# Performance work log

Measured on AMD Instinct MI355X. Metric: run time of the kernel, lower is better.

The kernel has to match this reference:

```python
import jax, jax.numpy as jnp
import numpy as np

N_AGENTS = 512
OBS = 128          # embed_fc_input_size (args.obs_space)
INP = 656          # input_shape
HID = 64           # rnn_hidden_dim
LAT = 256          # latent_dim (hard-coded)
NH = 64            # NN_HIDDEN_SIZE (hard-coded)
VAR_FLOOR = 0.002
KL_W = 1e-4
H_W = 1e-4
SOFT_W = 1.0
BN_EPS = 1e-5
LOG2PI = float(np.log(2.0 * np.pi))


def _bn(x, g, b, axis):
    # BatchNorm1d in training mode: biased batch stats over `axis`
    m = x.mean(axis=axis, keepdims=True)
    v = x.var(axis=axis, keepdims=True)
    return g * (x - m) / jnp.sqrt(v + BN_EPS) + b


def setup_inputs() -> dict:
    key = jax.random.key(0)
    ks = jax.random.split(key, 12)
    s = 0.02  # small init so exp(log-var head) stays tame
    p = {}
    p["obs"] = jax.random.normal(ks[0], (N_AGENTS, INP), jnp.float32)
    p["hidden_state"] = jax.random.normal(ks[1], (N_AGENTS, HID), jnp.float32)
    p["eps"] = jax.random.normal(ks[2], (N_AGENTS, LAT), jnp.float32)

    def lin(k, din, dout):
        return jax.random.normal(k, (din, dout), jnp.float32) * s, jnp.zeros((dout,), jnp.float32)

    # embed_net: Linear(OBS,64) -> BN -> LeakyReLU -> Linear(64, 2*LAT)
    p["eW1"], p["eb1"] = lin(ks[3], OBS, NH)
    p["eg"], p["ebt"] = jnp.ones((NH,), jnp.float32), jnp.zeros((NH,), jnp.float32)
    p["eW2"], p["eb2"] = lin(ks[4], NH, 2 * LAT)
    # inference_net: Linear(HID+INP,64) -> BN -> LeakyReLU -> Linear(64, 2*LAT)
    p["iW1"], p["ib1"] = lin(ks[5], HID + INP, NH)
    p["ig"], p["ibt"] = jnp.ones((NH,), jnp.float32), jnp.zeros((NH,), jnp.float32)
    p["iW2"], p["ib2"] = lin(ks[6], NH, 2 * LAT)
    # dis_net: Linear(2*LAT,64) -> BN -> LeakyReLU -> Linear(64,1)
    p["dW1"], p["db1"] = lin(ks[7], 2 * LAT, NH)
    p["dg"], p["dbt"] = jnp.ones((NH,), jnp.float32), jnp.zeros((NH,), jnp.float32)
    p["dW2"], p["db2"] = lin(ks[8], NH, 1)
    return p


def reference(obs, hidden_state, eps,
              eW1, eb1, eg, ebt, eW2, eb2,
              iW1, ib1, ig, ibt, iW2, ib2,
              dW1, db1, dg, dbt, dW2, db2):
    n = N_AGENTS  # bs == 1 is hard-coded in the module
    # --- embed_net ---
    emb_in = obs[:, -OBS:]
    h = jax.nn.leaky_relu(_bn(emb_in @ eW1 + eb1, eg, ebt, axis=0))
    lat = h @ eW2 + eb2                       # [n, 2*LAT]
    mu = lat[:, :LAT]
    var = jnp.maximum(jnp.exp(lat[:, LAT:]), VAR_FLOOR)
    sig = jnp.sqrt(var)
    latent = mu + sig * eps                   # rsample

    # --- inference_net (h_in detached) ---
    inf_in = jnp.concatenate([jax.lax.stop_gradient(hidden_state), obs], axis=1)
    hi = jax.nn.leaky_relu(_bn(inf_in @ iW1 + ib1, ig, ibt, axis=0))
    li = hi @ iW2 + ib2
    mu_q = li[:, :LAT]
    var_q = jnp.maximum(jnp.exp(li[:, LAT:]), VAR_FLOOR)
    sig_q = jnp.sqrt(var_q)

    entropy = (0.5 + 0.5 * LOG2PI + jnp.log(sig)).sum(-1).mean()
    kl = (jnp.log(sig_q / sig) + (var + (mu - mu_q) ** 2) / (2.0 * var_q) - 0.5).sum(-1).mean()
    loss0 = jnp.minimum(entropy * H_W + kl * KL_W, 2000.0)
    ce_loss = jnp.log1p(jnp.exp(loss0))

    # --- vectorized ring-shift pairwise pass (replaces n_agents Python loop) ---
    shifts = jnp.arange(1, n + 1)                        # loop iterations 1..n
    idx = (jnp.arange(n)[None, :] - shifts[:, None]) % n  # [n_shifts, n]
    moved = latent[idx]                                   # [S, n, LAT]

    # mi: per-dim Normal(mu_j, sig_j).log_prob of shifted latents
    logp = -((moved - mu[None]) ** 2) / (2.0 * var[None]) - jnp.log(sig)[None] - 0.5 * LOG2PI
    mi = jnp.maximum(logp + 13.9, -13.9).sum(-1) / LAT    # [S, n]

    # dis_net on concat(latent_j, moved_{s,j}); BN stats per shift iteration (batch = n)
    pair = jnp.concatenate([jnp.broadcast_to(latent[None], (n, n, LAT)), moved], axis=-1)
    h1 = pair @ dW1 + db1                                 # [S, n, NH]
    h1 = jax.nn.leaky_relu(_bn(h1, dg, dbt, axis=1))
    dis = jnp.abs(h1 @ dW2 + db2)[..., 0]                 # [S, n]

    mi_cat = mi.reshape(1, -1)                            # shift-major, matches cat order
    dis_cat = dis.reshape(1, -1)

    mi_n = (mi_cat - mi_cat.min(1, keepdims=True)) / (mi_cat.max(1, keepdims=True) - mi_cat.min(1, keepdims=True) + 1e-12)
    dis_n = (dis_cat - dis_cat.min(1, keepdims=True)) / (dis_cat.max(1, keepdims=True) - dis_cat.min(1, keepdims=True) + 1e-12)

    dis_loss = -jnp.minimum(mi_n + dis_n, 1.0).sum() / n  # / bs / n_agents, bs=1
    dis_norm = jnp.abs(dis_n).sum(axis=1).sum() / n
    c_dis_loss = (dis_norm + SOFT_W * dis_loss) / n
    loss = ce_loss + c_dis_loss
    return loss, c_dis_loss, ce_loss
```

## Files before the change

### kernel.cpp

```cpp
#include <hip/hip_runtime.h>

#define LOG2PI_F 1.8378770664093453f

#define W_ENC_PRE 0
#define W_INF_PRE 32768
#define W_ACC     65536
#define W_FIN     65792
#define W_MIMM    65796
#define W_DSMM    66308
#define W_ENT     67332
#define W_KL      67588
#define W_LATENT  67844
#define W_RPC     198916
#define W_A       723204
#define W_B       755972
#define W_AT      788740
#define W_BT      821508
#define W_ALPHA   854276
#define W_BETA    887044
#define W_MI      919812
#define W_DIS     1181956

__global__ __launch_bounds__(256) void k_pre(
    const float* __restrict__ obs, const float* __restrict__ hid,
    const float* __restrict__ eW1, const float* __restrict__ iW1,
    float* __restrict__ enc_pre, float* __restrict__ inf_pre,
    float* __restrict__ acc) {
  __shared__ float x[2][720];
  __shared__ float pi[4][2][64];
  __shared__ float pe[4][2][64];
  const int t = threadIdx.x;
  const int i0 = blockIdx.x * 2;
#pragma unroll
  for (int r = 0; r < 2; ++r)
    for (int k = t; k < 720; k += 256)
      x[r][k] = (k < 64) ? hid[(i0 + r) * 64 + k] : obs[(i0 + r) * 656 + (k - 64)];
  __syncthreads();
  const int c = t & 63, q = t >> 6;
  {
    float a0 = 0.f, a1 = 0.f;
    const int k0 = q * 180;
    for (int k = k0; k < k0 + 180; ++k) {
      const float w = iW1[k * 64 + c];
      a0 = fmaf(x[0][k], w, a0);
      a1 = fmaf(x[1][k], w, a1);
    }
    pi[q][0][c] = a0;
    pi[q][1][c] = a1;
  }
  {
    float a0 = 0.f, a1 = 0.f;
    const int k0 = q * 32;
    for (int k = k0; k < k0 + 32; ++k) {
      const float w = eW1[k * 64 + c];
      a0 = fmaf(x[0][592 + k], w, a0);
      a1 = fmaf(x[1][592 + k], w, a1);
    }
    pe[q][0][c] = a0;
    pe[q][1][c] = a1;
  }
  __syncthreads();
  if (t < 128) {
    const int r = t >> 6, c2 = t & 63;
    const float s = pi[0][r][c2] + pi[1][r][c2] + pi[2][r][c2] + pi[3][r][c2];
    inf_pre[(i0 + r) * 64 + c2] = s;
    atomicAdd(&acc[128 + c2], s);
    atomicAdd(&acc[192 + c2], s * s);
  } else {
    const int r = (t >> 6) & 1, c2 = t & 63;
    const float s = pe[0][r][c2] + pe[1][r][c2] + pe[2][r][c2] + pe[3][r][c2];
    enc_pre[(i0 + r) * 64 + c2] = s;
    atomicAdd(&acc[c2], s);
    atomicAdd(&acc[64 + c2], s * s);
  }
}

__global__ __launch_bounds__(256) void k_lat(
    const float* __restrict__ enc_pre, const float* __restrict__ inf_pre,
    const float* __restrict__ acc, const float* __restrict__ eg,
    const float* __restrict__ ebt, const float* __restrict__ ig,
    const float* __restrict__ ibt, const float* __restrict__ eW2,
    const float* __restrict__ eb2, const float* __restrict__ iW2,
    const float* __restrict__ ib2, const float* __restrict__ eps,
    float* __restrict__ latent, float* __restrict__ rpc,
    float* __restrict__ ent_part, float* __restrict__ kl_part) {
  __shared__ float sc[2][64], sh[2][64];
  __shared__ float h[2][2][64];
  __shared__ float red[256];
  const int t = threadIdx.x;
  const int i0 = blockIdx.x * 2;
  if (t < 128) {
    const int w = t >> 6, c = t & 63;
    const float sum = acc[w * 128 + c], sq = acc[w * 128 + 64 + c];
    const float mean = sum * (1.f / 512.f);
    float var = sq * (1.f / 512.f) - mean * mean;
    var = fmaxf(var, 0.f);
    const float g = w ? ig[c] : eg[c];
    const float bt = w ? ibt[c] : ebt[c];
    const float scale = g * rsqrtf(var + 1e-5f);
    sc[w][c] = scale;
    sh[w][c] = bt - mean * scale;
  }
  __syncthreads();
  {
    const int w = t >> 7, r = (t >> 6) & 1, c = t & 63;
    const float* pre = w ? inf_pre : enc_pre;
    const float v = fmaf(pre[(i0 + r) * 64 + c], sc[w][c], sh[w][c]);
    h[w][r][c] = (v >= 0.f) ? v : 0.01f * v;
  }
  __syncthreads();
  float me[2] = {0.f, 0.f}, ve[2] = {0.f, 0.f};
  float mq[2] = {0.f, 0.f}, vq[2] = {0.f, 0.f};
  for (int c = 0; c < 64; ++c) {
    const float we1 = eW2[c * 512 + t], we2 = eW2[c * 512 + 256 + t];
    const float wi1 = iW2[c * 512 + t], wi2 = iW2[c * 512 + 256 + t];
#pragma unroll
    for (int r = 0; r < 2; ++r) {
      me[r] = fmaf(h[0][r][c], we1, me[r]);
      ve[r] = fmaf(h[0][r][c], we2, ve[r]);
      mq[r] = fmaf(h[1][r][c], wi1, mq[r]);
      vq[r] = fmaf(h[1][r][c], wi2, vq[r]);
    }
  }
  const float ebm = eb2[t], ebv = eb2[256 + t];
  const float ibm = ib2[t], ibv = ib2[256 + t];
  float ent_l = 0.f, kl_l = 0.f;
#pragma unroll
  for (int r = 0; r < 2; ++r) {
    const int i = i0 + r;
    const float m = me[r] + ebm;
    const float var = fmaxf(expf(ve[r] + ebv), 0.002f);
    const float lse = 0.5f * logf(var);
    const float sig = sqrtf(var);
    const float mqq = mq[r] + ibm;
    const float varq = fmaxf(expf(vq[r] + ibv), 0.002f);
    const float lsq = 0.5f * logf(varq);
    latent[i * 256 + t] = fmaf(sig, eps[i * 256 + t], m);
    const float r_ = sqrtf(0.5f / var);
    float4 o;
    o.x = r_;
    o.y = m * r_;
    o.z = 13.9f - 0.5f * LOG2PI_F - lse;
    o.w = 0.f;
    *(float4*)&rpc[(i * 256 + t) * 4] = o;
    ent_l += 0.5f + 0.5f * LOG2PI_F + lse;
    const float dmu = m - mqq;
    kl_l += lsq - lse + (var + dmu * dmu) * (0.5f / varq) - 0.5f;
  }
  red[t] = ent_l;
  __syncthreads();
  for (int o = 128; o; o >>= 1) {
    if (t < o) red[t] += red[t + o];
    __syncthreads();
  }
  if (t == 0) ent_part[blockIdx.x] = red[0];
  __syncthreads();
  red[t] = kl_l;
  __syncthreads();
  for (int o = 128; o; o >>= 1) {
    if (t < o) red[t] += red[t + o];
    __syncthreads();
  }
  if (t == 0) kl_part[blockIdx.x] = red[0];
}

__global__ __launch_bounds__(256) void k_AB(
    const float* __restrict__ latent, const float* __restrict__ dW1,
    float* __restrict__ A, float* __restrict__ B, float* __restrict__ At,
    float* __restrict__ Bt, float* __restrict__ fin) {
  if (blockIdx.x == 0 && threadIdx.x == 0) {
    fin[0] = 0.f;
    fin[1] = 0.f;
    ((unsigned*)fin)[2] = 0u;
  }
  __shared__ float ls[2][256];
  __shared__ float pA[4][2][64], pB[4][2][64];
  const int t = threadIdx.x;
  const int j0 = blockIdx.x * 2;
  ls[0][t] = latent[j0 * 256 + t];
  ls[1][t] = latent[(j0 + 1) * 256 + t];
  __syncthreads();
  const int c = t & 63, q = t >> 6;
  float aA0 = 0.f, aA1 = 0.f, aB0 = 0.f, aB1 = 0.f;
  const int k0 = q * 64;
  for (int k = k0; k < k0 + 64; ++k) {
    const float wA = dW1[k * 64 + c];
    const float wB = dW1[(256 + k) * 64 + c];
    aA0 = fmaf(ls[0][k], wA, aA0);
    aA1 = fmaf(ls[1][k], wA, aA1);
    aB0 = fmaf(ls[0][k], wB, aB0);
    aB1 = fmaf(ls[1][k], wB, aB1);
  }
  pA[q][0][c] = aA0;
  pA[q][1][c] = aA1;
  pB[q][0][c] = aB0;
  pB[q][1][c] = aB1;
  __syncthreads();
  if (t < 128) {
    const int r = t >> 6, c2 = t & 63;
    const float s = pA[0][r][c2] + pA[1][r][c2] + pA[2][r][c2] + pA[3][r][c2];
    A[(j0 + r) * 64 + c2] = s;
    At[c2 * 512 + j0 + r] = s;
  } else {
    const int r = (t >> 6) & 1, c2 = t & 63;
    const float s = pB[0][r][c2] + pB[1][r][c2] + pB[2][r][c2] + pB[3][r][c2];
    B[(j0 + r) * 64 + c2] = s;
    Bt[c2 * 512 + j0 + r] = s;
  }
}

__global__ __launch_bounds__(256) void k_cross(
    const float* __restrict__ At, const float* __restrict__ Bt,
    const float* __restrict__ dg, const float* __restrict__ dbt,
    float* __restrict__ alpha, float* __restrict__ beta) {
  __shared__ float a[512], bb[512];
  __shared__ float red[256];
  __shared__ float pc[4][64];
  const int t = threadIdx.x;
  const int c = blockIdx.x >> 3;
  const int s0 = (blockIdx.x & 7) * 64;
  const float a0 = At[c * 512 + t], a1 = At[c * 512 + 256 + t];
  const float b0 = Bt[c * 512 + t], b1 = Bt[c * 512 + 256 + t];
  a[t] = a0;
  a[t + 256] = a1;
  bb[t] = b0;
  bb[t + 256] = b1;
  red[t] = a0 + a1 + b0 + b1;
  __syncthreads();
  for (int o = 128; o; o >>= 1) {
    if (t < o) red[t] += red[t + o];
    __syncthreads();
  }
  const float S = red[0];
  __syncthreads();
  red[t] = a0 * a0 + a1 * a1 + b0 * b0 + b1 * b1;
  __syncthreads();
  for (int o = 128; o; o >>= 1) {
    if (t < o) red[t] += red[t + o];
    __syncthreads();
  }
  const float Q = red[0];
  const int sl = t & 63, part = t >> 6;
  const int s = s0 + sl;
  float cr = 0.f;
  for (int j = part * 128; j < part * 128 + 128; ++j)
    cr = fmaf(a[j], bb[(j - s - 1) & 511], cr);
  pc[part][sl] = cr;
  __syncthreads();
  if (t < 64) {
    const int ss = s0 + t;
    const float cross = pc[0][t] + pc[1][t] + pc[2][t] + pc[3][t];
    const float mean = S * (1.f / 512.f);
    const float var = (Q + 2.f * cross) * (1.f / 512.f) - mean * mean;
    const float gc = dg[c], bc = dbt[c];
    const float al = rsqrtf(var + 1e-5f) * gc;
    alpha[ss * 64 + c] = al;
    beta[ss * 64 + c] = bc - mean * al;
  }
}

__global__ __launch_bounds__(256) void k_mi(
    const float* __restrict__ latent, const float* __restrict__ rpc,
    float* __restrict__ mi, float2* __restrict__ miMM) {
  __shared__ float lats[64][65];
  __shared__ float rpcs[16 * 256];
  __shared__ float mt[64][17];
  __shared__ float fmn[256], fmx[256];
  const int t = threadIdx.x;
  const int jt = blockIdx.x & 31, pt = blockIdx.x >> 5;
  const int j0 = jt * 16, p0 = pt * 64;
  const int pl = t & 31, jg = t >> 5;
  float regL[16], regR[16];
#pragma unroll
  for (int i = 0; i < 16; ++i) {
    const int idx = t + i * 256;
    regL[i] = latent[(p0 + (idx >> 6)) * 256 + (idx & 63)];
    regR[i] = rpc[(j0 + (idx >> 8)) * 1024 + (idx & 255)];
  }
  float a00 = 0.f, a01 = 0.f, a10 = 0.f, a11 = 0.f;
  for (int kc = 0; kc < 4; ++kc) {
    __syncthreads();
#pragma unroll
    for (int i = 0; i < 16; ++i) {
      const int idx = t + i * 256;
      lats[idx >> 6][idx & 63] = regL[i];
      rpcs[idx] = regR[i];
    }
    __syncthreads();
    if (kc < 3) {
#pragma unroll
      for (int i = 0; i < 16; ++i) {
        const int idx = t + i * 256;
        regL[i] = latent[(p0 + (idx >> 6)) * 256 + (kc + 1) * 64 + (idx & 63)];
        regR[i] = rpc[(j0 + (idx >> 8)) * 1024 + (kc + 1) * 256 + (idx & 255)];
      }
    }
    const float4* rp0 = (const float4*)&rpcs[(jg * 2) * 256];
    const float4* rp1 = (const float4*)&rpcs[(jg * 2 + 1) * 256];
#pragma unroll 8
    for (int k = 0; k < 64; ++k) {
      const float l0 = lats[pl][k], l1 = lats[pl + 32][k];
      const float4 r0 = rp0[k];
      const float4 r1 = rp1[k];
      float v;
      v = fmaf(l0, r0.x, -r0.y);
      a00 += fmaxf(fmaf(-v, v, r0.z), -13.9f);
      v = fmaf(l1, r0.x, -r0.y);
      a01 += fmaxf(fmaf(-v, v, r0.z), -13.9f);
      v = fmaf(l0, r1.x, -r1.y);
      a10 += fmaxf(fmaf(-v, v, r1.z), -13.9f);
      v = fmaf(l1, r1.x, -r1.y);
      a11 += fmaxf(fmaf(-v, v, r1.z), -13.9f);
    }
  }
  a00 *= (1.f / 256.f);
  a01 *= (1.f / 256.f);
  a10 *= (1.f / 256.f);
  a11 *= (1.f / 256.f);
  __syncthreads();
  mt[pl][jg * 2] = a00;
  mt[pl + 32][jg * 2] = a01;
  mt[pl][jg * 2 + 1] = a10;
  mt[pl + 32][jg * 2 + 1] = a11;
  fmn[t] = fminf(fminf(a00, a01), fminf(a10, a11));
  fmx[t] = fmaxf(fmaxf(a00, a01), fmaxf(a10, a11));
  __syncthreads();
  for (int o = 128; o; o >>= 1) {
    if (t < o) {
      fmn[t] = fminf(fmn[t], fmn[t + o]);
      fmx[t] = fmaxf(fmx[t], fmx[t + o]);
    }
    __syncthreads();
  }
  if (t == 0) miMM[blockIdx.x] = make_float2(fmn[0], fmx[0]);
  for (int i = t; i < 1024; i += 256) {
    const int pr = i >> 4, jc = i & 15;
    mi[(p0 + pr) * 512 + (j0 + jc)] = mt[pr][jc];
  }
}

__global__ __launch_bounds__(256) void k_dis(
    const float* __restrict__ A, const float* __restrict__ B,
    const float* __restrict__ alpha, const float* __restrict__ beta,
    const float* __restrict__ dW2, const float* __restrict__ db2,
    float* __restrict__ dis, float2* __restrict__ dsMM) {
  __shared__ float As[8 * 66];
  __shared__ float Bs[64 * 66];
  __shared__ float als[71 * 66];
  __shared__ float bes[71 * 66];
  __shared__ float w2s[64];
  __shared__ float dt[64][9];
  __shared__ float fmn[256], fmx[256];
  const int t = threadIdx.x;
  const int jt = blockIdx.x & 63, pt = blockIdx.x >> 6;
  const int j0 = jt * 8, p0 = pt * 64;
  for (int idx = t; idx < 8 * 64; idx += 256)
    As[(idx >> 6) * 66 + (idx & 63)] = A[(j0 + (idx >> 6)) * 64 + (idx & 63)];
  for (int idx = t; idx < 64 * 64; idx += 256)
    Bs[(idx >> 6) * 66 + (idx & 63)] = B[(p0 + (idx >> 6)) * 64 + (idx & 63)];
  for (int idx = t; idx < 71 * 64; idx += 256) {
    const int r = idx >> 6, c = idx & 63;
    const int s = (j0 - p0 - 64 + r) & 511;
    als[r * 66 + c] = alpha[s * 64 + c];
    bes[r * 66 + c] = beta[s * 64 + c];
  }
  if (t < 64) w2s[t] = dW2[t];
  const float db2v = db2[0];
  __syncthreads();
  const int pl = t & 31, jg = t >> 5;
  const int rb0 = jg - pl + 63;
  const int rb1 = jg - pl + 31;
  float acc0 = 0.f, acc1 = 0.f;
  for (int c = 0; c < 64; c += 2) {
    const float2 av = *(const float2*)&As[jg * 66 + c];
    const float2 bv0 = *(const float2*)&Bs[pl * 66 + c];
    const float2 bv1 = *(const float2*)&Bs[(pl + 32) * 66 + c];
    const float2 al0 = *(const float2*)&als[rb0 * 66 + c];
    const float2 al1 = *(const float2*)&als[rb1 * 66 + c];
    const float2 be0 = *(const float2*)&bes[rb0 * 66 + c];
    const float2 be1 = *(const float2*)&bes[rb1 * 66 + c];
    const float2 w = *(const float2*)&w2s[c];
    float v;
    v = fmaf(av.x + bv0.x, al0.x, be0.x);
    v = (v >= 0.f) ? v : 0.01f * v;
    acc0 = fmaf(v, w.x, acc0);
    v = fmaf(av.y + bv0.y, al0.y, be0.y);
    v = (v >= 0.f) ? v : 0.01f * v;
    acc0 = fmaf(v, w.y, acc0);
    v = fmaf(av.x + bv1.x, al1.x, be1.x);
    v = (v >= 0.f) ? v : 0.01f * v;
    acc1 = fmaf(v, w.x, acc1);
    v = fmaf(av.y + bv1.y, al1.y, be1.y);
    v = (v >= 0.f) ? v : 0.01f * v;
    acc1 = fmaf(v, w.y, acc1);
  }
  acc0 = fabsf(acc0 + db2v);
  acc1 = fabsf(acc1 + db2v);
  dt[pl][jg] = acc0;
  dt[pl + 32][jg] = acc1;
  fmn[t] = fminf(acc0, acc1);
  fmx[t] = fmaxf(acc0, acc1);
  __syncthreads();
  for (int o = 128; o; o >>= 1) {
    if (t < o) {
      fmn[t] = fminf(fmn[t], fmn[t + o]);
      fmx[t] = fmaxf(fmx[t], fmx[t + o]);
    }
    __syncthreads();
  }
  if (t == 0) dsMM[blockIdx.x] = make_float2(fmn[0], fmx[0]);
  for (int idx = t; idx < 512; idx += 256) {
    const int pr = idx >> 3, jc = idx & 7;
    dis[(p0 + pr) * 512 + (j0 + jc)] = dt[pr][jc];
  }
}

__global__ __launch_bounds__(256) void k_sumfin(
    const float* __restrict__ mi, const float* __restrict__ dis,
    const float2* __restrict__ miMM, const float2* __restrict__ dsMM,
    float* __restrict__ fin, const float* __restrict__ ent_part,
    const float* __restrict__ kl_part, float* __restrict__ out) {
  __shared__ float red1[256], red2[256], red3[256], red4[256];
  __shared__ int lastflag;
  const int t = threadIdx.x;
  {
    const float2 v = miMM[t];
    const float2 w0 = dsMM[t], w1 = dsMM[t + 256];
    red1[t] = v.x;
    red2[t] = v.y;
    red3[t] = fminf(w0.x, w1.x);
    red4[t] = fmaxf(w0.y, w1.y);
  }
  __syncthreads();
  for (int o = 128; o; o >>= 1) {
    if (t < o) {
      red1[t] = fminf(red1[t], red1[t + o]);
      red2[t] = fmaxf(red2[t], red2[t + o]);
      red3[t] = fminf(red3[t], red3[t + o]);
      red4[t] = fmaxf(red4[t], red4[t + o]);
    }
    __syncthreads();
  }
  const float mi_mn = red1[0], mi_mx = red2[0];
  const float d_mn = red3[0], d_mx = red4[0];
  __syncthreads();
  const float inv_mi = 1.f / (mi_mx - mi_mn + 1e-12f);
  const float inv_d = 1.f / (d_mx - d_mn + 1e-12f);
  float s1 = 0.f, s2 = 0.f;
  for (int i = blockIdx.x * 256 + t; i < 512 * 512; i += 65536) {
    const float mn_ = (mi[i] - mi_mn) * inv_mi;
    const float dn_ = (dis[i] - d_mn) * inv_d;
    s1 += fminf(mn_ + dn_, 1.0f);
    s2 += dn_;
  }
  red1[t] = s1;
  red2[t] = s2;
  __syncthreads();
  for (int o = 128; o; o >>= 1) {
    if (t < o) {
      red1[t] += red1[t + o];
      red2[t] += red2[t + o];
    }
    __syncthreads();
  }
  if (t == 0) {
    atomicAdd(&fin[0], red1[0]);
    atomicAdd(&fin[1], red2[0]);
    __threadfence();
    const unsigned old = atomicAdd((unsigned*)&fin[2], 1u);
    lastflag = (old == 255u) ? 1 : 0;
  }
  __syncthreads();
  if (!lastflag) return;
  red1[t] = ent_part[t];
  red2[t] = kl_part[t];
  __syncthreads();
  for (int o = 128; o; o >>= 1) {
    if (t < o) {
      red1[t] += red1[t + o];
      red2[t] += red2[t + o];
    }
    __syncthreads();
  }
  if (t == 0) {
    const float S1 = atomicAdd(&fin[0], 0.f);
    const float S2 = atomicAdd(&fin[1], 0.f);
    const double entropy = (double)red1[0] / 512.0;
    const double kl = (double)red2[0] / 512.0;
    double l0 = entropy * 1e-4 + kl * 1e-4;
    if (l0 > 2000.0) l0 = 2000.0;
    const double ce = log1p(exp(l0));
    const double dis_loss = -(double)S1 / 512.0;
    const double dis_norm = (double)S2 / 512.0;
    const double c_dis = (dis_norm + dis_loss) / 512.0;
    out[0] = (float)(ce + c_dis);
    out[1] = (float)c_dis;
    out[2] = (float)ce;
  }
}

extern "C" void kernel_launch(void* const* d_in, const int* in_sizes, int n_in,
                              void* d_out, int out_size, void* d_ws,
                              size_t ws_size, hipStream_t stream) {
  (void)in_sizes;
  (void)n_in;
  (void)out_size;
  (void)ws_size;
  const float* obs = (const float*)d_in[0];
  const float* hid = (const float*)d_in[1];
  const float* eps = (const float*)d_in[2];
  const float* eW1 = (const float*)d_in[3];
  const float* eg = (const float*)d_in[5];
  const float* ebt = (const float*)d_in[6];
  const float* eW2 = (const float*)d_in[7];
  const float* eb2 = (const float*)d_in[8];
  const float* iW1 = (const float*)d_in[9];
  const float* ig = (const float*)d_in[11];
  const float* ibt = (const float*)d_in[12];
  const float* iW2 = (const float*)d_in[13];
  const float* ib2 = (const float*)d_in[14];
  const float* dW1 = (const float*)d_in[15];
  const float* dg = (const float*)d_in[17];
  const float* dbt = (const float*)d_in[18];
  const float* dW2 = (const float*)d_in[19];
  const float* db2 = (const float*)d_in[20];
  float* ws = (float*)d_ws;
  float* out = (float*)d_out;

  hipMemsetAsync(ws + W_ACC, 0, 256 * sizeof(float), stream);

  k_pre<<<256, 256, 0, stream>>>(obs, hid, eW1, iW1, ws + W_ENC_PRE,
                                 ws + W_INF_PRE, ws + W_ACC);
  k_lat<<<256, 256, 0, stream>>>(ws + W_ENC_PRE, ws + W_INF_PRE, ws + W_ACC, eg,
                                 ebt, ig, ibt, eW2, eb2, iW2, ib2, eps,
                                 ws + W_LATENT, ws + W_RPC, ws + W_ENT,
                                 ws + W_KL);
  k_AB<<<256, 256, 0, stream>>>(ws + W_LATENT, dW1, ws + W_A, ws + W_B,
                                ws + W_AT, ws + W_BT, ws + W_FIN);
  k_cross<<<512, 256, 0, stream>>>(ws + W_AT, ws + W_BT, dg, dbt, ws + W_ALPHA,
                                   ws + W_BETA);
  k_mi<<<256, 256, 0, stream>>>(ws + W_LATENT, ws + W_RPC, ws + W_MI,
                                (float2*)(ws + W_MIMM));
  k_dis<<<512, 256, 0, stream>>>(ws + W_A, ws + W_B, ws + W_ALPHA, ws + W_BETA,
                                 dW2, db2, ws + W_DIS, (float2*)(ws + W_DSMM));
  k_sumfin<<<256, 256, 0, stream>>>(ws + W_MI, ws + W_DIS,
                                    (const float2*)(ws + W_MIMM),
                                    (const float2*)(ws + W_DSMM), ws + W_FIN,
                                    ws + W_ENT, ws + W_KL, out);
}
```

Baseline: 201.2 us.

## Replace BN stat atomics with per-block partials and merge mi/dis kernels

The first-layer BatchNorm statistics no longer go through global atomics on a memset-zeroed buffer. Each k_pre block now writes its own partial sums and sums of squares, and every k_lat block reduces all 256 partials itself. The independent mi and dis kernels are merged into one 768-block launch that picks its branch by block index and shares one carved-up shared-memory buffer. This drops a memset, the atomic contention and one kernel launch, and lets both workloads fill the GPU together. The cost is that each k_lat block now makes 256 redundant strided reads, and the merged kernel's shared-memory footprint is sized for the larger branch, which may limit occupancy.

```diff
diff --git a/kernel.cpp b/kernel.cpp
--- a/kernel.cpp
+++ b/kernel.cpp
@@ -4,7 +4,6 @@
 
 #define W_ENC_PRE 0
 #define W_INF_PRE 32768
-#define W_ACC     65536
 #define W_FIN     65792
 #define W_MIMM    65796
 #define W_DSMM    66308
@@ -20,17 +19,20 @@
 #define W_BETA    887044
 #define W_MI      919812
 #define W_DIS     1181956
+#define W_PACC    1446144
 
 __global__ __launch_bounds__(256) void k_pre(
     const float* __restrict__ obs, const float* __restrict__ hid,
     const float* __restrict__ eW1, const float* __restrict__ iW1,
     float* __restrict__ enc_pre, float* __restrict__ inf_pre,
-    float* __restrict__ acc) {
+    float* __restrict__ pacc) {
   __shared__ float x[2][720];
   __shared__ float pi[4][2][64];
   __shared__ float pe[4][2][64];
+  __shared__ float sb[256];
   const int t = threadIdx.x;
-  const int i0 = blockIdx.x * 2;
+  const int vb = blockIdx.x;
+  const int i0 = vb * 2;
 #pragma unroll
   for (int r = 0; r < 2; ++r)
     for (int k = t; k < 720; k += 256)
@@ -60,38 +62,54 @@
     pe[q][1][c] = a1;
   }
   __syncthreads();
+  float s;
   if (t < 128) {
     const int r = t >> 6, c2 = t & 63;
-    const float s = pi[0][r][c2] + pi[1][r][c2] + pi[2][r][c2] + pi[3][r][c2];
+    s = pi[0][r][c2] + pi[1][r][c2] + pi[2][r][c2] + pi[3][r][c2];
     inf_pre[(i0 + r) * 64 + c2] = s;
-    atomicAdd(&acc[128 + c2], s);
-    atomicAdd(&acc[192 + c2], s * s);
   } else {
     const int r = (t >> 6) & 1, c2 = t & 63;
-    const float s = pe[0][r][c2] + pe[1][r][c2] + pe[2][r][c2] + pe[3][r][c2];
+    s = pe[0][r][c2] + pe[1][r][c2] + pe[2][r][c2] + pe[3][r][c2];
     enc_pre[(i0 + r) * 64 + c2] = s;
-    atomicAdd(&acc[c2], s);
-    atomicAdd(&acc[64 + c2], s * s);
+  }
+  sb[t] = s;
+  __syncthreads();
+  if (t < 64) {
+    const float e0 = sb[128 + t], e1 = sb[192 + t];
+    pacc[vb * 256 + t] = e0 + e1;
+    pacc[vb * 256 + 64 + t] = e0 * e0 + e1 * e1;
+  } else if (t < 128) {
+    const int c2 = t - 64;
+    const float v0 = sb[c2], v1 = sb[64 + c2];
+    pacc[vb * 256 + 128 + c2] = v0 + v1;
+    pacc[vb * 256 + 192 + c2] = v0 * v0 + v1 * v1;
   }
 }
 
 __global__ __launch_bounds__(256) void k_lat(
     const float* __restrict__ enc_pre, const float* __restrict__ inf_pre,
-    const float* __restrict__ acc, const float* __restrict__ eg,
+    const float* __restrict__ pacc, const float* __restrict__ eg,
     const float* __restrict__ ebt, const float* __restrict__ ig,
     const float* __restrict__ ibt, const float* __restrict__ eW2,
     const float* __restrict__ eb2, const float* __restrict__ iW2,
     const float* __restrict__ ib2, const float* __restrict__ eps,
     float* __restrict__ latent, float* __restrict__ rpc,
     float* __restrict__ ent_part, float* __restrict__ kl_part) {
+  __shared__ float sval[256];
   __shared__ float sc[2][64], sh[2][64];
   __shared__ float h[2][2][64];
   __shared__ float red[256];
   const int t = threadIdx.x;
   const int i0 = blockIdx.x * 2;
+  {
+    float v = 0.f;
+    for (int b = 0; b < 256; ++b) v += pacc[b * 256 + t];
+    sval[t] = v;
+  }
+  __syncthreads();
   if (t < 128) {
     const int w = t >> 6, c = t & 63;
-    const float sum = acc[w * 128 + c], sq = acc[w * 128 + 64 + c];
+    const float sum = sval[w * 128 + c], sq = sval[w * 128 + 64 + c];
     const float mean = sum * (1.f / 512.f);
     float var = sq * (1.f / 512.f) - mean * mean;
     var = fmaxf(var, 0.f);
@@ -259,159 +277,163 @@
   }
 }
 
-__global__ __launch_bounds__(256) void k_mi(
+__global__ __launch_bounds__(256) void k_midis(
     const float* __restrict__ latent, const float* __restrict__ rpc,
-    float* __restrict__ mi, float2* __restrict__ miMM) {
-  __shared__ float lats[64][65];
-  __shared__ float rpcs[16 * 256];
-  __shared__ float mt[64][17];
-  __shared__ float fmn[256], fmx[256];
+    const float* __restrict__ A, const float* __restrict__ B,
+    const float* __restrict__ alpha, const float* __restrict__ beta,
+    const float* __restrict__ dW2, const float* __restrict__ db2,
+    float* __restrict__ mi, float* __restrict__ dis,
+    float2* __restrict__ miMM, float2* __restrict__ dsMM) {
+  __shared__ __align__(16) float sm[15276];
   const int t = threadIdx.x;
-  const int jt = blockIdx.x & 31, pt = blockIdx.x >> 5;
-  const int j0 = jt * 16, p0 = pt * 64;
-  const int pl = t & 31, jg = t >> 5;
-  float regL[16], regR[16];
-#pragma unroll
-  for (int i = 0; i < 16; ++i) {
-    const int idx = t + i * 256;
-    regL[i] = latent[(p0 + (idx >> 6)) * 256 + (idx & 63)];
-    regR[i] = rpc[(j0 + (idx >> 8)) * 1024 + (idx & 255)];
-  }
-  float a00 = 0.f, a01 = 0.f, a10 = 0.f, a11 = 0.f;
-  for (int kc = 0; kc < 4; ++kc) {
-    __syncthreads();
+  if (blockIdx.x < 256) {
+    float* lats = sm;
+    float* rpcs = sm + 4160;
+    float* mt = sm + 8256;
+    float* fmn = sm + 9344;
+    float* fmx = sm + 9600;
+    const int vb = blockIdx.x;
+    const int jt = vb & 31, pt = vb >> 5;
+    const int j0 = jt * 16, p0 = pt * 64;
+    const int pl = t & 31, jg = t >> 5;
+    float regL[16], regR[16];
 #pragma unroll
     for (int i = 0; i < 16; ++i) {
       const int idx = t + i * 256;
-      lats[idx >> 6][idx & 63] = regL[i];
-      rpcs[idx] = regR[i];
-    }
-    __syncthreads();
-    if (kc < 3) {
+      regL[i] = latent[(p0 + (idx >> 6)) * 256 + (idx & 63)];
+      regR[i] = rpc[(j0 + (idx >> 8)) * 1024 + (idx & 255)];
+    }
+    float a00 = 0.f, a01 = 0.f, a10 = 0.f, a11 = 0.f;
+    for (int kc = 0; kc < 4; ++kc) {
+      __syncthreads();
 #pragma unroll
       for (int i = 0; i < 16; ++i) {
         const int idx = t + i * 256;
-        regL[i] = latent[(p0 + (idx >> 6)) * 256 + (kc + 1) * 64 + (idx & 63)];
-        regR[i] = rpc[(j0 + (idx >> 8)) * 1024 + (kc + 1) * 256 + (idx & 255)];
+        lats[(idx >> 6) * 65 + (idx & 63)] = regL[i];
+        rpcs[idx] = regR[i];
       }
-    }
-    const float4* rp0 = (const float4*)&rpcs[(jg * 2) * 256];
-    const float4* rp1 = (const float4*)&rpcs[(jg * 2 + 1) * 256];
+      __syncthreads();
+      if (kc < 3) {
+#pragma unroll
+        for (int i = 0; i < 16; ++i) {
+          const int idx = t + i * 256;
+          regL[i] = latent[(p0 + (idx >> 6)) * 256 + (kc + 1) * 64 + (idx & 63)];
+          regR[i] = rpc[(j0 + (idx >> 8)) * 1024 + (kc + 1) * 256 + (idx & 255)];
+        }
+      }
+      const float4* rp0 = (const float4*)&rpcs[(jg * 2) * 256];
+      const float4* rp1 = (const float4*)&rpcs[(jg * 2 + 1) * 256];
 #pragma unroll 8
-    for (int k = 0; k < 64; ++k) {
-      const float l0 = lats[pl][k], l1 = lats[pl + 32][k];
-      const float4 r0 = rp0[k];
-      const float4 r1 = rp1[k];
+      for (int k = 0; k < 64; ++k) {
+        const float l0 = lats[pl * 65 + k], l1 = lats[(pl + 32) * 65 + k];
+        const float4 r0 = rp0[k];
+        const float4 r1 = rp1[k];
+        float v;
+        v = fmaf(l0, r0.x, -r0.y);
+        a00 += fmaxf(fmaf(-v, v, r0.z), -13.9f);
+        v = fmaf(l1, r0.x, -r0.y);
+        a01 += fmaxf(fmaf(-v, v, r0.z), -13.9f);
+        v = fmaf(l0, r1.x, -r1.y);
+        a10 += fmaxf(fmaf(-v, v, r1.z), -13.9f);
+        v = fmaf(l1, r1.x, -r1.y);
+        a11 += fmaxf(fmaf(-v, v, r1.z), -13.9f);
+      }
+    }
+    a00 *= (1.f / 256.f);
+    a01 *= (1.f / 256.f);
+    a10 *= (1.f / 256.f);
+    a11 *= (1.f / 256.f);
+    __syncthreads();
+    mt[pl * 17 + jg * 2] = a00;
+    mt[(pl + 32) * 17 + jg * 2] = a01;
+    mt[pl * 17 + jg * 2 + 1] = a10;
+    mt[(pl + 32) * 17 + jg * 2 + 1] = a11;
+    fmn[t] = fminf(fminf(a00, a01), fminf(a10, a11));
+    fmx[t] = fmaxf(fmaxf(a00, a01), fmaxf(a10, a11));
+    __syncthreads();
+    for (int o = 128; o; o >>= 1) {
+      if (t < o) {
+        fmn[t] = fminf(fmn[t], fmn[t + o]);
+        fmx[t] = fmaxf(fmx[t], fmx[t + o]);
+      }
+      __syncthreads();
+    }
+    if (t == 0) miMM[vb] = make_float2(fmn[0], fmx[0]);
+    for (int i = t; i < 1024; i += 256) {
+      const int pr = i >> 4, jc = i & 15;
+      mi[(p0 + pr) * 512 + (j0 + jc)] = mt[pr * 17 + jc];
+    }
+  } else {
+    float* As = sm;
+    float* Bs = sm + 528;
+    float* als = sm + 4752;
+    float* bes = sm + 9438;
+    float* w2s = sm + 14124;
+    float* dt = sm + 14188;
+    float* fmn = sm + 14764;
+    float* fmx = sm + 15020;
+    const int vb = blockIdx.x - 256;
+    const int jt = vb & 63, pt = vb >> 6;
+    const int j0 = jt * 8, p0 = pt * 64;
+    for (int idx = t; idx < 8 * 64; idx += 256)
+      As[(idx >> 6) * 66 + (idx & 63)] = A[(j0 + (idx >> 6)) * 64 + (idx & 63)];
+    for (int idx = t; idx < 64 * 64; idx += 256)
+      Bs[(idx >> 6) * 66 + (idx & 63)] = B[(p0 + (idx >> 6)) * 64 + (idx & 63)];
+    for (int idx = t; idx < 71 * 64; idx += 256) {
+      const int r = idx >> 6, c = idx & 63;
+      const int s = (j0 - p0 - 64 + r) & 511;
+      als[r * 66 + c] = alpha[s * 64 + c];
+      bes[r * 66 + c] = beta[s * 64 + c];
+    }
+    if (t < 64) w2s[t] = dW2[t];
+    const float db2v = db2[0];
+    __syncthreads();
+    const int pl = t & 31, jg = t >> 5;
+    const int rb0 = jg - pl + 63;
+    const int rb1 = jg - pl + 31;
+    float acc0 = 0.f, acc1 = 0.f;
+    for (int c = 0; c < 64; c += 2) {
+      const float2 av = *(const float2*)&As[jg * 66 + c];
+      const float2 bv0 = *(const float2*)&Bs[pl * 66 + c];
+      const float2 bv1 = *(const float2*)&Bs[(pl + 32) * 66 + c];
+      const float2 al0 = *(const float2*)&als[rb0 * 66 + c];
+      const float2 al1 = *(const float2*)&als[rb1 * 66 + c];
+      const float2 be0 = *(const float2*)&bes[rb0 * 66 + c];
+      const float2 be1 = *(const float2*)&bes[rb1 * 66 + c];
+      const float2 w = *(const float2*)&w2s[c];
       float v;
-      v = fmaf(l0, r0.x, -r0.y);
-      a00 += fmaxf(fmaf(-v, v, r0.z), -13.9f);
-      v = fmaf(l1, r0.x, -r0.y);
-      a01 += fmaxf(fmaf(-v, v, r0.z), -13.9f);
-      v = fmaf(l0, r1.x, -r1.y);
-      a10 += fmaxf(fmaf(-v, v, r1.z), -13.9f);
-      v = fmaf(l1, r1.x, -r1.y);
-      a11 += fmaxf(fmaf(-v, v, r1.z), -13.9f);
-    }
-  }
-  a00 *= (1.f / 256.f);
-  a01 *= (1.f / 256.f);
-  a10 *= (1.f / 256.f);
-  a11 *= (1.f / 256.f);
-  __syncthreads();
-  mt[pl][jg * 2] = a00;
-  mt[pl + 32][jg * 2] = a01;
-  mt[pl][jg * 2 + 1] = a10;
-  mt[pl + 32][jg * 2 + 1] = a11;
-  fmn[t] = fminf(fminf(a00, a01), fminf(a10, a11));
-  fmx[t] = fmaxf(fmaxf(a00, a01), fmaxf(a10, a11));
-  __syncthreads();
-  for (int o = 128; o; o >>= 1) {
-    if (t < o) {
-      fmn[t] = fminf(fmn[t], fmn[t + o]);
-      fmx[t] = fmaxf(fmx[t], fmx[t + o]);
-    }
-    __syncthreads();
-  }
-  if (t == 0) miMM[blockIdx.x] = make_float2(fmn[0], fmx[0]);
-  for (int i = t; i < 1024; i += 256) {
-    const int pr = i >> 4, jc = i & 15;
-    mi[(p0 + pr) * 512 + (j0 + jc)] = mt[pr][jc];
-  }
-}
-
-__global__ __launch_bounds__(256) void k_dis(
-    const float* __restrict__ A, const float* __restrict__ B,
-    const float* __restrict__ alpha, const float* __restrict__ beta,
-    const float* __restrict__ dW2, const float* __restrict__ db2,
-    float* __restrict__ dis, float2* __restrict__ dsMM) {
-  __shared__ float As[8 * 66];
-  __shared__ float Bs[64 * 66];
-  __shared__ float als[71 * 66];
-  __shared__ float bes[71 * 66];
-  __shared__ float w2s[64];
-  __shared__ float dt[64][9];
-  __shared__ float fmn[256], fmx[256];
-  const int t = threadIdx.x;
-  const int jt = blockIdx.x & 63, pt = blockIdx.x >> 6;
-  const int j0 = jt * 8, p0 = pt * 64;
-  for (int idx = t; idx < 8 * 64; idx += 256)
-    As[(idx >> 6) * 66 + (idx & 63)] = A[(j0 + (idx >> 6)) * 64 + (idx & 63)];
-  for (int idx = t; idx < 64 * 64; idx += 256)
-    Bs[(idx >> 6) * 66 + (idx & 63)] = B[(p0 + (idx >> 6)) * 64 + (idx & 63)];
-  for (int idx = t; idx < 71 * 64; idx += 256) {
-    const int r = idx >> 6, c = idx & 63;
-    const int s = (j0 - p0 - 64 + r) & 511;
-    als[r * 66 + c] = alpha[s * 64 + c];
-    bes[r * 66 + c] = beta[s * 64 + c];
-  }
-  if (t < 64) w2s[t] = dW2[t];
-  const float db2v = db2[0];
-  __syncthreads();
-  const int pl = t & 31, jg = t >> 5;
-  const int rb0 = jg - pl + 63;
-  const int rb1 = jg - pl + 31;
-  float acc0 = 0.f, acc1 = 0.f;
-  for (int c = 0; c < 64; c += 2) {
-    const float2 av = *(const float2*)&As[jg * 66 + c];
-    const float2 bv0 = *(const float2*)&Bs[pl * 66 + c];
-    const float2 bv1 = *(const float2*)&Bs[(pl + 32) * 66 + c];
-    const float2 al0 = *(const float2*)&als[rb0 * 66 + c];
-    const float2 al1 = *(const float2*)&als[rb1 * 66 + c];
-    const float2 be0 = *(const float2*)&bes[rb0 * 66 + c];
-    const float2 be1 = *(const float2*)&bes[rb1 * 66 + c];
-    const float2 w = *(const float2*)&w2s[c];
-    float v;
-    v = fmaf(av.x + bv0.x, al0.x, be0.x);
-    v = (v >= 0.f) ? v : 0.01f * v;
-    acc0 = fmaf(v, w.x, acc0);
-    v = fmaf(av.y + bv0.y, al0.y, be0.y);
-    v = (v >= 0.f) ? v : 0.01f * v;
-    acc0 = fmaf(v, w.y, acc0);
-    v = fmaf(av.x + bv1.x, al1.x, be1.x);
-    v = (v >= 0.f) ? v : 0.01f * v;
-    acc1 = fmaf(v, w.x, acc1);
-    v = fmaf(av.y + bv1.y, al1.y, be1.y);
-    v = (v >= 0.f) ? v : 0.01f * v;
-    acc1 = fmaf(v, w.y, acc1);
-  }
-  acc0 = fabsf(acc0 + db2v);
-  acc1 = fabsf(acc1 + db2v);
-  dt[pl][jg] = acc0;
-  dt[pl + 32][jg] = acc1;
-  fmn[t] = fminf(acc0, acc1);
-  fmx[t] = fmaxf(acc0, acc1);
-  __syncthreads();
-  for (int o = 128; o; o >>= 1) {
-    if (t < o) {
-      fmn[t] = fminf(fmn[t], fmn[t + o]);
-      fmx[t] = fmaxf(fmx[t], fmx[t + o]);
-    }
-    __syncthreads();
-  }
-  if (t == 0) dsMM[blockIdx.x] = make_float2(fmn[0], fmx[0]);
-  for (int idx = t; idx < 512; idx += 256) {
-    const int pr = idx >> 3, jc = idx & 7;
-    dis[(p0 + pr) * 512 + (j0 + jc)] = dt[pr][jc];
+      v = fmaf(av.x + bv0.x, al0.x, be0.x);
+      v = (v >= 0.f) ? v : 0.01f * v;
+      acc0 = fmaf(v, w.x, acc0);
+      v = fmaf(av.y + bv0.y, al0.y, be0.y);
+      v = (v >= 0.f) ? v : 0.01f * v;
+      acc0 = fmaf(v, w.y, acc0);
+      v = fmaf(av.x + bv1.x, al1.x, be1.x);
+      v = (v >= 0.f) ? v : 0.01f * v;
+      acc1 = fmaf(v, w.x, acc1);
+      v = fmaf(av.y + bv1.y, al1.y, be1.y);
+      v = (v >= 0.f) ? v : 0.01f * v;
+      acc1 = fmaf(v, w.y, acc1);
+    }
+    acc0 = fabsf(acc0 + db2v);
+    acc1 = fabsf(acc1 + db2v);
+    dt[pl * 9 + jg] = acc0;
+    dt[(pl + 32) * 9 + jg] = acc1;
+    fmn[t] = fminf(acc0, acc1);
+    fmx[t] = fmaxf(acc0, acc1);
+    __syncthreads();
+    for (int o = 128; o; o >>= 1) {
+      if (t < o) {
+        fmn[t] = fminf(fmn[t], fmn[t + o]);
+        fmx[t] = fmaxf(fmx[t], fmx[t + o]);
+      }
+      __syncthreads();
+    }
+    if (t == 0) dsMM[vb] = make_float2(fmn[0], fmx[0]);
+    for (int idx = t; idx < 512; idx += 256) {
+      const int pr = idx >> 3, jc = idx & 7;
+      dis[(p0 + pr) * 512 + (j0 + jc)] = dt[pr * 9 + jc];
+    }
   }
 }
 
@@ -527,22 +549,21 @@
   float* ws = (float*)d_ws;
   float* out = (float*)d_out;
 
-  hipMemsetAsync(ws + W_ACC, 0, 256 * sizeof(float), stream);
-
   k_pre<<<256, 256, 0, stream>>>(obs, hid, eW1, iW1, ws + W_ENC_PRE,
-                                 ws + W_INF_PRE, ws + W_ACC);
-  k_lat<<<256, 256, 0, stream>>>(ws + W_ENC_PRE, ws + W_INF_PRE, ws + W_ACC, eg,
-                                 ebt, ig, ibt, eW2, eb2, iW2, ib2, eps,
+                                 ws + W_INF_PRE, ws + W_PACC);
+  k_lat<<<256, 256, 0, stream>>>(ws + W_ENC_PRE, ws + W_INF_PRE, ws + W_PACC,
+                                 eg, ebt, ig, ibt, eW2, eb2, iW2, ib2, eps,
                                  ws + W_LATENT, ws + W_RPC, ws + W_ENT,
                                  ws + W_KL);
   k_AB<<<256, 256, 0, stream>>>(ws + W_LATENT, dW1, ws + W_A, ws + W_B,
                                 ws + W_AT, ws + W_BT, ws + W_FIN);
   k_cross<<<512, 256, 0, stream>>>(ws + W_AT, ws + W_BT, dg, dbt, ws + W_ALPHA,
                                    ws + W_BETA);
-  k_mi<<<256, 256, 0, stream>>>(ws + W_LATENT, ws + W_RPC, ws + W_MI,
-                                (float2*)(ws + W_MIMM));
-  k_dis<<<512, 256, 0, stream>>>(ws + W_A, ws + W_B, ws + W_ALPHA, ws + W_BETA,
-                                 dW2, db2, ws + W_DIS, (float2*)(ws + W_DSMM));
+  k_midis<<<768, 256, 0, stream>>>(ws + W_LATENT, ws + W_RPC, ws + W_A,
+                                   ws + W_B, ws + W_ALPHA, ws + W_BETA, dW2,
+                                   db2, ws + W_MI, ws + W_DIS,
+                                   (float2*)(ws + W_MIMM),
+                                   (float2*)(ws + W_DSMM));
   k_sumfin<<<256, 256, 0, stream>>>(ws + W_MI, ws + W_DIS,
                                     (const float2*)(ws + W_MIMM),
                                     (const float2*)(ws + W_DSMM), ws + W_FIN,
```

After: 184.7 us. 1.09x faster.
